# Kernel tuning notes

Measured on AMD Instinct MI355X. Metric: run time of the kernel, lower is better.

## Reference

```python
import jax, jax.numpy as jnp
import numpy as np

R, B, S, H, E = 8, 8, 512, 768, 64


def setup_inputs() -> dict:
    key = jax.random.key(0)
    ks = jax.random.split(key, 9)
    return {
        "role_labels": jax.random.uniform(ks[0], (R, B, S), dtype=jnp.float32),
        "summar_role_embedding": jax.random.normal(ks[1], (R, B, S, H), dtype=jnp.float32),
        "token_embedding": jax.random.normal(ks[2], (B, S, H), dtype=jnp.float32),
        "entities_embedding": jax.random.normal(ks[3], (B, S, H), dtype=jnp.float32),
        "token_mask": jnp.ones((B, S), jnp.float32),
        "entity2token": jax.random.randint(ks[4], (B, S), 0, E, dtype=jnp.int32),
        "token2entity": jax.random.randint(ks[5], (B, S), 0, E, dtype=jnp.int32),
        "W_single": jax.random.normal(ks[6], (3 * H, 1), dtype=jnp.float32) * 0.02,
        "b_single": jnp.zeros((1,), jnp.float32),
        "W_multi": jax.random.normal(ks[7], (3 * H, 1), dtype=jnp.float32) * 0.02,
        "b_multi": jnp.zeros((1,), jnp.float32),
        "W_ans": jax.random.normal(ks[8], (2 * H, H), dtype=jnp.float32) * 0.02,
        "b_ans": jnp.zeros((H,), jnp.float32),
    }


def reference(role_labels, summar_role_embedding, token_embedding, entities_embedding,
              token_mask, entity2token, token2entity,
              W_single, b_single, W_multi, b_multi, W_ans, b_ans):
    Bn = token_embedding.shape[0]
    # flattened segment ids: batch b, entity e -> b*E + e
    seg = (jnp.arange(Bn, dtype=entity2token.dtype)[:, None] * E + entity2token).reshape(-1)
    eps = 1e-7
    mask_sum = token_mask.sum()

    def step(carry, xs):
        pre_answer, loss = carry
        sr, labels = xs  # [B,S,H], [B,S]
        single = jax.nn.sigmoid(
            jnp.concatenate([sr, token_embedding, pre_answer], -1) @ W_single + b_single)[..., 0]
        multi = jax.nn.sigmoid(
            jnp.concatenate([sr, entities_embedding, pre_answer], -1) @ W_multi + b_multi)[..., 0]
        # per-(batch,entity) scatter-max of multi-word scores
        scores = jax.ops.segment_max(multi.reshape(-1), seg, num_segments=Bn * E).reshape(Bn, E)
        scores = jnp.maximum(scores, 0.0)  # entity_scores initialized to 0 in original
        # broadcast entity score back to its token span positions
        pred_ent = jnp.take_along_axis(scores, token2entity.astype(jnp.int32), axis=1)
        merged = jnp.maximum(single, pred_ent)  # [B,S]
        curr_answer = token_embedding * merged[..., None]
        pre_next = jnp.concatenate([curr_answer, pre_answer], -1) @ W_ans + b_ans
        p = jnp.clip(merged, eps, 1.0 - eps)
        bce = -(labels * jnp.log(p) + (1.0 - labels) * jnp.log1p(-p)).mean()
        loss = loss + bce * mask_sum  # (BCE-mean scalar * mask).sum() == bce * mask.sum()
        return (pre_next, loss), merged

    init = (jnp.zeros_like(token_embedding), jnp.asarray(0.0, jnp.float32))
    (_, total_loss), logits = jax.lax.scan(step, init, (summar_role_embedding, role_labels))
    return total_loss, logits  # scalar, [R,B,S]
```

## Files before the change

### kernel.cpp

```cpp
#include <hip/hip_runtime.h>
#include <math.h>

#define HD   768
#define NR   8
#define NB   8
#define SL   512
#define NE   64
#define NTOK 4096
#define NSR  32768

__device__ __forceinline__ float wred(float v) {
  #pragma unroll
  for (int m = 32; m >= 1; m >>= 1) v += __shfl_xor(v, m, 64);
  return v;
}

__device__ __forceinline__ float dot12(const float4 a0, const float4 a1, const float4 a2,
                                       const float* __restrict__ w, int lane) {
  const float4 w0 = *reinterpret_cast<const float4*>(w + lane * 4);
  const float4 w1 = *reinterpret_cast<const float4*>(w + 256 + lane * 4);
  const float4 w2 = *reinterpret_cast<const float4*>(w + 512 + lane * 4);
  float s = 0.f;
  s = fmaf(a0.x, w0.x, s); s = fmaf(a0.y, w0.y, s); s = fmaf(a0.z, w0.z, s); s = fmaf(a0.w, w0.w, s);
  s = fmaf(a1.x, w1.x, s); s = fmaf(a1.y, w1.y, s); s = fmaf(a1.z, w1.z, s); s = fmaf(a1.w, w1.w, s);
  s = fmaf(a2.x, w2.x, s); s = fmaf(a2.y, w2.y, s); s = fmaf(a2.z, w2.z, s); s = fmaf(a2.w, w2.w, s);
  return s;
}

__global__ __launch_bounds__(256) void chain_kernel(
    const float* __restrict__ W_ans, const float* __restrict__ b_ans,
    const float* __restrict__ uS_in, const float* __restrict__ uM_in,
    float* __restrict__ vS_out, float* __restrict__ vM_out,
    float* __restrict__ uS_out, float* __restrict__ uM_out,
    float* __restrict__ buS, float* __restrict__ buM)
{
  const int wid  = blockIdx.x * 4 + (threadIdx.x >> 6);
  const int lane = threadIdx.x & 63;
  if (wid < 3072) {
    const int cm  = (wid >= 1536);
    const int row = wid - (cm ? 1536 : 0);
    const float* u = cm ? uM_in : uS_in;
    const float* wr = W_ans + (size_t)row * HD;
    const float4 a0 = *reinterpret_cast<const float4*>(wr + lane * 4);
    const float4 a1 = *reinterpret_cast<const float4*>(wr + 256 + lane * 4);
    const float4 a2 = *reinterpret_cast<const float4*>(wr + 512 + lane * 4);
    float acc = wred(dot12(a0, a1, a2, u, lane));
    if (lane == 0) {
      if (row < HD) { (cm ? vM_out : vS_out)[row] = acc; }
      else          { (cm ? uM_out : uS_out)[row - HD] = acc; }
    }
  } else if (wid < 3074) {
    const float* u = (wid == 3073) ? uM_in : uS_in;
    const float4 a0 = *reinterpret_cast<const float4*>(b_ans + lane * 4);
    const float4 a1 = *reinterpret_cast<const float4*>(b_ans + 256 + lane * 4);
    const float4 a2 = *reinterpret_cast<const float4*>(b_ans + 512 + lane * 4);
    float acc = wred(dot12(a0, a1, a2, u, lane));
    if (lane == 0) { if (wid == 3073) *buM = acc; else *buS = acc; }
  }
}

__global__ __launch_bounds__(256) void dots_kernel(
    const float* __restrict__ sr, const float* __restrict__ tok, const float* __restrict__ ent,
    const float* __restrict__ Wsing, const float* __restrict__ Wmult,
    const float* __restrict__ vS, const float* __restrict__ vM,
    float* __restrict__ as_out, float* __restrict__ am_out,
    float* __restrict__ ps_out, float* __restrict__ pm_out,
    float* __restrict__ dts_out, float* __restrict__ dem_out)
{
  const int wid  = blockIdx.x * 4 + (threadIdx.x >> 6);
  const int lane = threadIdx.x & 63;
  if (wid < NSR) {
    const float* row = sr + (size_t)wid * HD;
    const float4 x0 = *reinterpret_cast<const float4*>(row + lane * 4);
    const float4 x1 = *reinterpret_cast<const float4*>(row + 256 + lane * 4);
    const float4 x2 = *reinterpret_cast<const float4*>(row + 512 + lane * 4);
    float aS = wred(dot12(x0, x1, x2, Wsing, lane));
    float aM = wred(dot12(x0, x1, x2, Wmult, lane));
    if (lane == 0) { as_out[wid] = aS; am_out[wid] = aM; }
  } else if (wid < NSR + NTOK) {
    const int t = wid - NSR;
    const float* tr = tok + (size_t)t * HD;
    const float* er = ent + (size_t)t * HD;
    const float4 t0 = *reinterpret_cast<const float4*>(tr + lane * 4);
    const float4 t1 = *reinterpret_cast<const float4*>(tr + 256 + lane * 4);
    const float4 t2 = *reinterpret_cast<const float4*>(tr + 512 + lane * 4);
    const float4 e0 = *reinterpret_cast<const float4*>(er + lane * 4);
    const float4 e1 = *reinterpret_cast<const float4*>(er + 256 + lane * 4);
    const float4 e2v = *reinterpret_cast<const float4*>(er + 512 + lane * 4);
    float dts = wred(dot12(t0, t1, t2, Wsing + HD, lane));
    float dem = wred(dot12(e0, e1, e2v, Wmult + HD, lane));
    float psv[7], pmv[7];
    #pragma unroll
    for (int k = 0; k < 7; ++k) {
      psv[k] = wred(dot12(t0, t1, t2, vS + k * HD, lane));
      pmv[k] = wred(dot12(t0, t1, t2, vM + k * HD, lane));
    }
    if (lane == 0) {
      dts_out[t] = dts; dem_out[t] = dem;
      #pragma unroll
      for (int k = 0; k < 7; ++k) { ps_out[k * NTOK + t] = psv[k]; pm_out[k * NTOK + t] = pmv[k]; }
    }
  }
}

__global__ __launch_bounds__(512) void step_kernel(
    const float* __restrict__ labels, const int* __restrict__ e2t, const int* __restrict__ t2e,
    const float* __restrict__ ps, const float* __restrict__ pm,
    const float* __restrict__ dts, const float* __restrict__ dem,
    const float* __restrict__ as_, const float* __restrict__ am_,
    const float* __restrict__ buS, const float* __restrict__ buM,
    const float* __restrict__ b_single, const float* __restrict__ b_multi,
    float* __restrict__ out, double* __restrict__ partial_bce)
{
  __shared__ unsigned sc[NR][NE];
  const int s = threadIdx.x;
  const int b = blockIdx.x;
  const int t = b * SL + s;
  reinterpret_cast<unsigned*>(sc)[s] = 0u;
  float psv[7], pmv[7], asv[8], amv[8], buSv[7], buMv[7];
  #pragma unroll
  for (int k = 0; k < 7; ++k) { psv[k] = ps[k * NTOK + t]; pmv[k] = pm[k * NTOK + t]; }
  #pragma unroll
  for (int r = 0; r < 8; ++r) { asv[r] = as_[r * NTOK + t]; amv[r] = am_[r * NTOK + t]; }
  #pragma unroll
  for (int k = 0; k < 7; ++k) { buSv[k] = buS[k]; buMv[k] = buM[k]; }
  const float dtsv = dts[t], demv = dem[t];
  const float b1 = b_single[0], b2 = b_multi[0];
  const int e2 = e2t[t] & (NE - 1);
  const int t2 = t2e[t] & (NE - 1);
  __syncthreads();

  float m[8];
  float cs = 0.f, cmv = 0.f;
  double bsum = 0.0;
  #pragma unroll
  for (int r = 0; r < 8; ++r) {
    float As = cs, Am = cmv;
    #pragma unroll
    for (int j = 0; j < r; ++j) {
      As = fmaf(m[j], psv[r - 1 - j], As);
      Am = fmaf(m[j], pmv[r - 1 - j], Am);
    }
    const float xs = asv[r] + dtsv + As + b1;
    const float xm = amv[r] + demv + Am + b2;
    const float sing = 1.f / (1.f + expf(-xs));
    const float mult = 1.f / (1.f + expf(-xm));
    atomicMax(&sc[r][e2], __float_as_uint(mult));
    __syncthreads();
    const float pred = __uint_as_float(sc[r][t2]);
    const float merged = fmaxf(sing, pred);
    m[r] = merged;
    out[1 + r * NTOK + t] = merged;
    const float lab = labels[r * NTOK + t];
    const float p = fminf(fmaxf(merged, 1e-7f), 1.0f - 1e-7f);
    bsum += (double)(-(lab * logf(p) + (1.f - lab) * log1pf(-p)));
    if (r < 7) { cs += buSv[r]; cmv += buMv[r]; }
  }
  #pragma unroll
  for (int off = 32; off >= 1; off >>= 1) bsum += __shfl_xor(bsum, off, 64);
  __shared__ double wsum[8];
  if ((threadIdx.x & 63) == 0) wsum[threadIdx.x >> 6] = bsum;
  __syncthreads();
  if (threadIdx.x == 0) {
    double tot = 0.0;
    #pragma unroll
    for (int i = 0; i < 8; ++i) tot += wsum[i];
    partial_bce[b] = tot;
  }
}

__global__ __launch_bounds__(256) void finalize_kernel(
    const float* __restrict__ mask, const double* __restrict__ partial_bce, float* __restrict__ out)
{
  const int tid = threadIdx.x;
  float sm = 0.f;
  for (int i = tid; i < NTOK; i += 256) sm += mask[i];
  sm = wred(sm);
  __shared__ float w4[4];
  if ((tid & 63) == 0) w4[tid >> 6] = sm;
  __syncthreads();
  if (tid == 0) {
    const float msum = w4[0] + w4[1] + w4[2] + w4[3];
    double tot = 0.0;
    #pragma unroll
    for (int i = 0; i < 8; ++i) tot += partial_bce[i];
    out[0] = (float)(tot * (double)msum / 4096.0);
  }
}

extern "C" void kernel_launch(void* const* d_in, const int* in_sizes, int n_in,
                              void* d_out, int out_size, void* d_ws, size_t ws_size,
                              hipStream_t stream) {
  (void)in_sizes; (void)n_in; (void)out_size; (void)ws_size;
  const float* labels = (const float*)d_in[0];
  const float* sr     = (const float*)d_in[1];
  const float* tok    = (const float*)d_in[2];
  const float* ent    = (const float*)d_in[3];
  const float* mask   = (const float*)d_in[4];
  const int*   e2t    = (const int*)d_in[5];
  const int*   t2e    = (const int*)d_in[6];
  const float* Wsing  = (const float*)d_in[7];
  const float* bsing  = (const float*)d_in[8];
  const float* Wmult  = (const float*)d_in[9];
  const float* bmult  = (const float*)d_in[10];
  const float* Wans   = (const float*)d_in[11];
  const float* bans   = (const float*)d_in[12];

  float* ws  = (float*)d_ws;
  float* uS  = ws;
  float* uM  = uS + 8 * HD;
  float* vS  = uM + 8 * HD;
  float* vM  = vS + 7 * HD;
  float* buS = vM + 7 * HD;
  float* buM = buS + 8;
  float* ps  = buM + 8;
  float* pm  = ps + 7 * NTOK;
  float* dts = pm + 7 * NTOK;
  float* dem = dts + NTOK;
  float* as_ = dem + NTOK;
  float* am_ = as_ + 8 * NTOK;
  double* pb = (double*)(am_ + 8 * NTOK);

  for (int k = 0; k < 7; ++k) {
    const float* uSin = (k == 0) ? (Wsing + 2 * HD) : (uS + k * HD);
    const float* uMin = (k == 0) ? (Wmult + 2 * HD) : (uM + k * HD);
    chain_kernel<<<769, 256, 0, stream>>>(Wans, bans, uSin, uMin,
        vS + k * HD, vM + k * HD, uS + (k + 1) * HD, uM + (k + 1) * HD,
        buS + k, buM + k);
  }
  dots_kernel<<<9216, 256, 0, stream>>>(sr, tok, ent, Wsing, Wmult, vS, vM,
        as_, am_, ps, pm, dts, dem);
  step_kernel<<<8, 512, 0, stream>>>(labels, e2t, t2e, ps, pm, dts, dem,
        as_, am_, buS, buM, bsing, bmult, (float*)d_out, pb);
  finalize_kernel<<<1, 256, 0, stream>>>(mask, pb, (float*)d_out);
}
```

Before: 234.7 us.

## Fuse all stages into one persistent kernel with grid barriers and overlapped sr dots

```diff
diff --git a/kernel.cpp b/kernel.cpp
--- a/kernel.cpp
+++ b/kernel.cpp
@@ -8,8 +8,26 @@
 #define NE   64
 #define NTOK 4096
 #define NSR  32768
+#define GRID 768
+#define NWAVES (GRID * 4)
+#define SRSLICE 4682
+#define C1N 16
+#define C1TARGET (GRID / C1N)
+
+struct Args {
+  const float *labels, *sr, *tok, *ent, *mask;
+  const int *e2t, *t2e;
+  const float *Wsing, *bsing, *Wmult, *bmult, *Wans, *bans;
+  float *ws;
+  float *out;
+};
 
 __device__ __forceinline__ float wred(float v) {
+  #pragma unroll
+  for (int m = 32; m >= 1; m >>= 1) v += __shfl_xor(v, m, 64);
+  return v;
+}
+__device__ __forceinline__ double wredd(double v) {
   #pragma unroll
   for (int m = 32; m >= 1; m >>= 1) v += __shfl_xor(v, m, 64);
   return v;
@@ -27,164 +45,196 @@
   return s;
 }
 
-__global__ __launch_bounds__(256) void chain_kernel(
-    const float* __restrict__ W_ans, const float* __restrict__ b_ans,
-    const float* __restrict__ uS_in, const float* __restrict__ uM_in,
-    float* __restrict__ vS_out, float* __restrict__ vM_out,
-    float* __restrict__ uS_out, float* __restrict__ uM_out,
-    float* __restrict__ buS, float* __restrict__ buM)
-{
-  const int wid  = blockIdx.x * 4 + (threadIdx.x >> 6);
-  const int lane = threadIdx.x & 63;
-  if (wid < 3072) {
-    const int cm  = (wid >= 1536);
-    const int row = wid - (cm ? 1536 : 0);
-    const float* u = cm ? uM_in : uS_in;
-    const float* wr = W_ans + (size_t)row * HD;
-    const float4 a0 = *reinterpret_cast<const float4*>(wr + lane * 4);
-    const float4 a1 = *reinterpret_cast<const float4*>(wr + 256 + lane * 4);
-    const float4 a2 = *reinterpret_cast<const float4*>(wr + 512 + lane * 4);
-    float acc = wred(dot12(a0, a1, a2, u, lane));
-    if (lane == 0) {
-      if (row < HD) { (cm ? vM_out : vS_out)[row] = acc; }
-      else          { (cm ? uM_out : uS_out)[row - HD] = acc; }
-    }
-  } else if (wid < 3074) {
-    const float* u = (wid == 3073) ? uM_in : uS_in;
-    const float4 a0 = *reinterpret_cast<const float4*>(b_ans + lane * 4);
-    const float4 a1 = *reinterpret_cast<const float4*>(b_ans + 256 + lane * 4);
-    const float4 a2 = *reinterpret_cast<const float4*>(b_ans + 512 + lane * 4);
-    float acc = wred(dot12(a0, a1, a2, u, lane));
-    if (lane == 0) { if (wid == 3073) *buM = acc; else *buS = acc; }
-  }
-}
-
-__global__ __launch_bounds__(256) void dots_kernel(
-    const float* __restrict__ sr, const float* __restrict__ tok, const float* __restrict__ ent,
-    const float* __restrict__ Wsing, const float* __restrict__ Wmult,
-    const float* __restrict__ vS, const float* __restrict__ vM,
-    float* __restrict__ as_out, float* __restrict__ am_out,
-    float* __restrict__ ps_out, float* __restrict__ pm_out,
-    float* __restrict__ dts_out, float* __restrict__ dem_out)
-{
-  const int wid  = blockIdx.x * 4 + (threadIdx.x >> 6);
-  const int lane = threadIdx.x & 63;
-  if (wid < NSR) {
-    const float* row = sr + (size_t)wid * HD;
-    const float4 x0 = *reinterpret_cast<const float4*>(row + lane * 4);
-    const float4 x1 = *reinterpret_cast<const float4*>(row + 256 + lane * 4);
-    const float4 x2 = *reinterpret_cast<const float4*>(row + 512 + lane * 4);
-    float aS = wred(dot12(x0, x1, x2, Wsing, lane));
-    float aM = wred(dot12(x0, x1, x2, Wmult, lane));
-    if (lane == 0) { as_out[wid] = aS; am_out[wid] = aM; }
-  } else if (wid < NSR + NTOK) {
-    const int t = wid - NSR;
-    const float* tr = tok + (size_t)t * HD;
-    const float* er = ent + (size_t)t * HD;
+__device__ __forceinline__ float rowdot(const float* __restrict__ a, const float* __restrict__ w, int lane) {
+  const float4 a0 = *reinterpret_cast<const float4*>(a + lane * 4);
+  const float4 a1 = *reinterpret_cast<const float4*>(a + 256 + lane * 4);
+  const float4 a2 = *reinterpret_cast<const float4*>(a + 512 + lane * 4);
+  return wred(dot12(a0, a1, a2, w, lane));
+}
+
+__device__ __forceinline__ void gridbar(unsigned* B, int bid, int tid) {
+  __syncthreads();
+  if (tid == 0) {
+    __threadfence();
+    unsigned* c1  = B + (bid & (C1N - 1)) * 32;
+    unsigned* c2  = B + 512;
+    unsigned* gen = B + 544;
+    unsigned g = __hip_atomic_load(gen, __ATOMIC_RELAXED, __HIP_MEMORY_SCOPE_AGENT);
+    bool done = false;
+    if (__hip_atomic_fetch_add(c1, 1u, __ATOMIC_ACQ_REL, __HIP_MEMORY_SCOPE_AGENT) == C1TARGET - 1) {
+      __hip_atomic_store(c1, 0u, __ATOMIC_RELAXED, __HIP_MEMORY_SCOPE_AGENT);
+      if (__hip_atomic_fetch_add(c2, 1u, __ATOMIC_ACQ_REL, __HIP_MEMORY_SCOPE_AGENT) == C1N - 1) {
+        __hip_atomic_store(c2, 0u, __ATOMIC_RELAXED, __HIP_MEMORY_SCOPE_AGENT);
+        __hip_atomic_fetch_add(gen, 1u, __ATOMIC_RELEASE, __HIP_MEMORY_SCOPE_AGENT);
+        done = true;
+      }
+    }
+    if (!done) {
+      while (__hip_atomic_load(gen, __ATOMIC_RELAXED, __HIP_MEMORY_SCOPE_AGENT) == g)
+        __builtin_amdgcn_s_sleep(2);
+    }
+    __threadfence();
+  }
+  __syncthreads();
+}
+
+__global__ void init_kernel(unsigned* B) {
+  for (int i = threadIdx.x; i < 640; i += 256) B[i] = 0u;
+}
+
+__global__ __launch_bounds__(256, 4) void fused_kernel(Args A) {
+  const int tid  = threadIdx.x;
+  const int lane = tid & 63;
+  const int bid  = blockIdx.x;
+  const int gwid = bid * 4 + (tid >> 6);
+
+  unsigned* B  = (unsigned*)A.ws;
+  float* F     = A.ws;
+  float* msum  = F + 640;
+  double* pbce = (double*)(F + 648);
+  float* uS  = F + 704;
+  float* uM  = uS + 8 * HD;
+  float* vS  = uM + 8 * HD;
+  float* vM  = vS + 7 * HD;
+  float* buS = vM + 7 * HD;
+  float* buM = buS + 8;
+  float* as_ = F + 24064;
+  float* am_ = as_ + NSR;
+  float* ps  = am_ + NSR;
+  float* pm  = ps + 7 * NTOK;
+  float* dts = pm + 7 * NTOK;
+  float* dem = dts + NTOK;
+
+  for (int p = 0; p < 7; ++p) {
+    if (gwid < 1536) {
+      const int cm  = gwid >= 768;
+      const int row = gwid & 767;
+      const float* u = (p == 0) ? ((cm ? A.Wmult : A.Wsing) + 2 * HD)
+                                : ((cm ? uM : uS) + p * HD);
+      if (p < 6) {
+        float acc = rowdot(A.Wans + (size_t)(HD + row) * HD, u, lane);
+        if (lane == 0) ((cm ? uM : uS) + (p + 1) * HD)[row] = acc;
+      }
+      if (row == 0) {
+        float bb = rowdot(A.bans, u, lane);
+        if (lane == 0) (cm ? buM : buS)[p] = bb;
+      }
+    } else if (gwid < 3072) {
+      const int cm  = gwid >= 2304;
+      const int row = gwid & 767;
+      const float* u = (p == 0) ? ((cm ? A.Wmult : A.Wsing) + 2 * HD)
+                                : ((cm ? uM : uS) + p * HD);
+      float acc = rowdot(A.Wans + (size_t)row * HD, u, lane);
+      if (lane == 0) ((cm ? vM : vS) + p * HD)[row] = acc;
+    }
+    if (p == 0 && gwid == 1600) {
+      const float4* m4 = (const float4*)A.mask;
+      float sm = 0.f;
+      for (int i = lane; i < NTOK / 4; i += 64) {
+        float4 v = m4[i];
+        sm += v.x + v.y + v.z + v.w;
+      }
+      sm = wred(sm);
+      if (lane == 0) *msum = sm;
+    }
+    const int e = ((p + 1) * SRSLICE < NSR) ? (p + 1) * SRSLICE : NSR;
+    for (int r = p * SRSLICE + gwid; r < e; r += NWAVES) {
+      const float* row = A.sr + (size_t)r * HD;
+      const float4 x0 = *reinterpret_cast<const float4*>(row + lane * 4);
+      const float4 x1 = *reinterpret_cast<const float4*>(row + 256 + lane * 4);
+      const float4 x2 = *reinterpret_cast<const float4*>(row + 512 + lane * 4);
+      float aS = wred(dot12(x0, x1, x2, A.Wsing, lane));
+      float aM = wred(dot12(x0, x1, x2, A.Wmult, lane));
+      if (lane == 0) { as_[r] = aS; am_[r] = aM; }
+    }
+    gridbar(B, bid, tid);
+  }
+
+  for (int t = gwid; t < NTOK; t += NWAVES) {
+    const float* tr = A.tok + (size_t)t * HD;
+    const float* er = A.ent + (size_t)t * HD;
     const float4 t0 = *reinterpret_cast<const float4*>(tr + lane * 4);
     const float4 t1 = *reinterpret_cast<const float4*>(tr + 256 + lane * 4);
     const float4 t2 = *reinterpret_cast<const float4*>(tr + 512 + lane * 4);
     const float4 e0 = *reinterpret_cast<const float4*>(er + lane * 4);
     const float4 e1 = *reinterpret_cast<const float4*>(er + 256 + lane * 4);
-    const float4 e2v = *reinterpret_cast<const float4*>(er + 512 + lane * 4);
-    float dts = wred(dot12(t0, t1, t2, Wsing + HD, lane));
-    float dem = wred(dot12(e0, e1, e2v, Wmult + HD, lane));
-    float psv[7], pmv[7];
+    const float4 e2 = *reinterpret_cast<const float4*>(er + 512 + lane * 4);
+    float dtsv = wred(dot12(t0, t1, t2, A.Wsing + HD, lane));
+    float demv = wred(dot12(e0, e1, e2, A.Wmult + HD, lane));
+    if (lane == 0) { dts[t] = dtsv; dem[t] = demv; }
     #pragma unroll
     for (int k = 0; k < 7; ++k) {
-      psv[k] = wred(dot12(t0, t1, t2, vS + k * HD, lane));
-      pmv[k] = wred(dot12(t0, t1, t2, vM + k * HD, lane));
-    }
-    if (lane == 0) {
-      dts_out[t] = dts; dem_out[t] = dem;
-      #pragma unroll
-      for (int k = 0; k < 7; ++k) { ps_out[k * NTOK + t] = psv[k]; pm_out[k * NTOK + t] = pmv[k]; }
-    }
-  }
-}
-
-__global__ __launch_bounds__(512) void step_kernel(
-    const float* __restrict__ labels, const int* __restrict__ e2t, const int* __restrict__ t2e,
-    const float* __restrict__ ps, const float* __restrict__ pm,
-    const float* __restrict__ dts, const float* __restrict__ dem,
-    const float* __restrict__ as_, const float* __restrict__ am_,
-    const float* __restrict__ buS, const float* __restrict__ buM,
-    const float* __restrict__ b_single, const float* __restrict__ b_multi,
-    float* __restrict__ out, double* __restrict__ partial_bce)
-{
+      float a = wred(dot12(t0, t1, t2, vS + k * HD, lane));
+      float b = wred(dot12(t0, t1, t2, vM + k * HD, lane));
+      if (lane == 0) { ps[k * NTOK + t] = a; pm[k * NTOK + t] = b; }
+    }
+  }
+  gridbar(B, bid, tid);
+
+  if (bid >= NB) return;
   __shared__ unsigned sc[NR][NE];
-  const int s = threadIdx.x;
-  const int b = blockIdx.x;
-  const int t = b * SL + s;
-  reinterpret_cast<unsigned*>(sc)[s] = 0u;
-  float psv[7], pmv[7], asv[8], amv[8], buSv[7], buMv[7];
-  #pragma unroll
-  for (int k = 0; k < 7; ++k) { psv[k] = ps[k * NTOK + t]; pmv[k] = pm[k * NTOK + t]; }
-  #pragma unroll
-  for (int r = 0; r < 8; ++r) { asv[r] = as_[r * NTOK + t]; amv[r] = am_[r * NTOK + t]; }
-  #pragma unroll
-  for (int k = 0; k < 7; ++k) { buSv[k] = buS[k]; buMv[k] = buM[k]; }
-  const float dtsv = dts[t], demv = dem[t];
-  const float b1 = b_single[0], b2 = b_multi[0];
-  const int e2 = e2t[t] & (NE - 1);
-  const int t2 = t2e[t] & (NE - 1);
-  __syncthreads();
-
-  float m[8];
+  __shared__ double wsumD[4];
+  const int b = bid;
+  const int t0 = b * SL + tid, t1 = t0 + 256;
+  reinterpret_cast<unsigned*>(sc)[tid] = 0u;
+  reinterpret_cast<unsigned*>(sc)[tid + 256] = 0u;
+  float ps0[7], pm0[7], ps1[7], pm1[7], buSv[7], buMv[7];
+  #pragma unroll
+  for (int k = 0; k < 7; ++k) {
+    ps0[k] = ps[k * NTOK + t0]; pm0[k] = pm[k * NTOK + t0];
+    ps1[k] = ps[k * NTOK + t1]; pm1[k] = pm[k * NTOK + t1];
+    buSv[k] = buS[k]; buMv[k] = buM[k];
+  }
+  const float dts0 = dts[t0], dem0 = dem[t0], dts1 = dts[t1], dem1 = dem[t1];
+  const float b1 = A.bsing[0], b2 = A.bmult[0];
+  const int e0i = A.e2t[t0] & (NE - 1), e1i = A.e2t[t1] & (NE - 1);
+  const int q0 = A.t2e[t0] & (NE - 1), q1 = A.t2e[t1] & (NE - 1);
+  __syncthreads();
+
+  float m0[8], m1[8];
   float cs = 0.f, cmv = 0.f;
   double bsum = 0.0;
   #pragma unroll
   for (int r = 0; r < 8; ++r) {
-    float As = cs, Am = cmv;
+    float As0 = cs, Am0 = cmv, As1 = cs, Am1 = cmv;
     #pragma unroll
     for (int j = 0; j < r; ++j) {
-      As = fmaf(m[j], psv[r - 1 - j], As);
-      Am = fmaf(m[j], pmv[r - 1 - j], Am);
-    }
-    const float xs = asv[r] + dtsv + As + b1;
-    const float xm = amv[r] + demv + Am + b2;
-    const float sing = 1.f / (1.f + expf(-xs));
-    const float mult = 1.f / (1.f + expf(-xm));
-    atomicMax(&sc[r][e2], __float_as_uint(mult));
+      As0 = fmaf(m0[j], ps0[r - 1 - j], As0); Am0 = fmaf(m0[j], pm0[r - 1 - j], Am0);
+      As1 = fmaf(m1[j], ps1[r - 1 - j], As1); Am1 = fmaf(m1[j], pm1[r - 1 - j], Am1);
+    }
+    const float sing0 = 1.f / (1.f + expf(-(as_[r * NTOK + t0] + dts0 + As0 + b1)));
+    const float mult0 = 1.f / (1.f + expf(-(am_[r * NTOK + t0] + dem0 + Am0 + b2)));
+    const float sing1 = 1.f / (1.f + expf(-(as_[r * NTOK + t1] + dts1 + As1 + b1)));
+    const float mult1 = 1.f / (1.f + expf(-(am_[r * NTOK + t1] + dem1 + Am1 + b2)));
+    atomicMax(&sc[r][e0i], __float_as_uint(mult0));
+    atomicMax(&sc[r][e1i], __float_as_uint(mult1));
     __syncthreads();
-    const float pred = __uint_as_float(sc[r][t2]);
-    const float merged = fmaxf(sing, pred);
-    m[r] = merged;
-    out[1 + r * NTOK + t] = merged;
-    const float lab = labels[r * NTOK + t];
-    const float p = fminf(fmaxf(merged, 1e-7f), 1.0f - 1e-7f);
-    bsum += (double)(-(lab * logf(p) + (1.f - lab) * log1pf(-p)));
+    const float mg0 = fmaxf(sing0, __uint_as_float(sc[r][q0]));
+    const float mg1 = fmaxf(sing1, __uint_as_float(sc[r][q1]));
+    m0[r] = mg0; m1[r] = mg1;
+    A.out[1 + r * NTOK + t0] = mg0;
+    A.out[1 + r * NTOK + t1] = mg1;
+    const float la0 = A.labels[r * NTOK + t0], la1 = A.labels[r * NTOK + t1];
+    const float p0 = fminf(fmaxf(mg0, 1e-7f), 1.f - 1e-7f);
+    const float p1 = fminf(fmaxf(mg1, 1e-7f), 1.f - 1e-7f);
+    bsum += (double)(-(la0 * logf(p0) + (1.f - la0) * log1pf(-p0)));
+    bsum += (double)(-(la1 * logf(p1) + (1.f - la1) * log1pf(-p1)));
     if (r < 7) { cs += buSv[r]; cmv += buMv[r]; }
   }
-  #pragma unroll
-  for (int off = 32; off >= 1; off >>= 1) bsum += __shfl_xor(bsum, off, 64);
-  __shared__ double wsum[8];
-  if ((threadIdx.x & 63) == 0) wsum[threadIdx.x >> 6] = bsum;
-  __syncthreads();
-  if (threadIdx.x == 0) {
-    double tot = 0.0;
-    #pragma unroll
-    for (int i = 0; i < 8; ++i) tot += wsum[i];
-    partial_bce[b] = tot;
-  }
-}
-
-__global__ __launch_bounds__(256) void finalize_kernel(
-    const float* __restrict__ mask, const double* __restrict__ partial_bce, float* __restrict__ out)
-{
-  const int tid = threadIdx.x;
-  float sm = 0.f;
-  for (int i = tid; i < NTOK; i += 256) sm += mask[i];
-  sm = wred(sm);
-  __shared__ float w4[4];
-  if ((tid & 63) == 0) w4[tid >> 6] = sm;
+  bsum = wredd(bsum);
+  if ((tid & 63) == 0) wsumD[tid >> 6] = bsum;
   __syncthreads();
   if (tid == 0) {
-    const float msum = w4[0] + w4[1] + w4[2] + w4[3];
-    double tot = 0.0;
-    #pragma unroll
-    for (int i = 0; i < 8; ++i) tot += partial_bce[i];
-    out[0] = (float)(tot * (double)msum / 4096.0);
+    pbce[b] = wsumD[0] + wsumD[1] + wsumD[2] + wsumD[3];
+    __threadfence();
+    unsigned k = atomicAdd(B + 576, 1u);
+    if (k == NB - 1) {
+      __threadfence();
+      double tot = 0.0;
+      #pragma unroll
+      for (int i = 0; i < 8; ++i) tot += ((volatile double*)pbce)[i];
+      A.out[0] = (float)(tot * (double)(*(volatile float*)msum) / 4096.0);
+    }
   }
 }
 
@@ -192,45 +242,22 @@
                               void* d_out, int out_size, void* d_ws, size_t ws_size,
                               hipStream_t stream) {
   (void)in_sizes; (void)n_in; (void)out_size; (void)ws_size;
-  const float* labels = (const float*)d_in[0];
-  const float* sr     = (const float*)d_in[1];
-  const float* tok    = (const float*)d_in[2];
-  const float* ent    = (const float*)d_in[3];
-  const float* mask   = (const float*)d_in[4];
-  const int*   e2t    = (const int*)d_in[5];
-  const int*   t2e    = (const int*)d_in[6];
-  const float* Wsing  = (const float*)d_in[7];
-  const float* bsing  = (const float*)d_in[8];
-  const float* Wmult  = (const float*)d_in[9];
-  const float* bmult  = (const float*)d_in[10];
-  const float* Wans   = (const float*)d_in[11];
-  const float* bans   = (const float*)d_in[12];
-
-  float* ws  = (float*)d_ws;
-  float* uS  = ws;
-  float* uM  = uS + 8 * HD;
-  float* vS  = uM + 8 * HD;
-  float* vM  = vS + 7 * HD;
-  float* buS = vM + 7 * HD;
-  float* buM = buS + 8;
-  float* ps  = buM + 8;
-  float* pm  = ps + 7 * NTOK;
-  float* dts = pm + 7 * NTOK;
-  float* dem = dts + NTOK;
-  float* as_ = dem + NTOK;
-  float* am_ = as_ + 8 * NTOK;
-  double* pb = (double*)(am_ + 8 * NTOK);
-
-  for (int k = 0; k < 7; ++k) {
-    const float* uSin = (k == 0) ? (Wsing + 2 * HD) : (uS + k * HD);
-    const float* uMin = (k == 0) ? (Wmult + 2 * HD) : (uM + k * HD);
-    chain_kernel<<<769, 256, 0, stream>>>(Wans, bans, uSin, uMin,
-        vS + k * HD, vM + k * HD, uS + (k + 1) * HD, uM + (k + 1) * HD,
-        buS + k, buM + k);
-  }
-  dots_kernel<<<9216, 256, 0, stream>>>(sr, tok, ent, Wsing, Wmult, vS, vM,
-        as_, am_, ps, pm, dts, dem);
-  step_kernel<<<8, 512, 0, stream>>>(labels, e2t, t2e, ps, pm, dts, dem,
-        as_, am_, buS, buM, bsing, bmult, (float*)d_out, pb);
-  finalize_kernel<<<1, 256, 0, stream>>>(mask, pb, (float*)d_out);
-}
+  Args a;
+  a.labels = (const float*)d_in[0];
+  a.sr     = (const float*)d_in[1];
+  a.tok    = (const float*)d_in[2];
+  a.ent    = (const float*)d_in[3];
+  a.mask   = (const float*)d_in[4];
+  a.e2t    = (const int*)d_in[5];
+  a.t2e    = (const int*)d_in[6];
+  a.Wsing  = (const float*)d_in[7];
+  a.bsing  = (const float*)d_in[8];
+  a.Wmult  = (const float*)d_in[9];
+  a.bmult  = (const float*)d_in[10];
+  a.Wans   = (const float*)d_in[11];
+  a.bans   = (const float*)d_in[12];
+  a.ws     = (float*)d_ws;
+  a.out    = (float*)d_out;
+  init_kernel<<<1, 256, 0, stream>>>((unsigned*)d_ws);
+  fused_kernel<<<GRID, 256, 0, stream>>>(a);
+}
```

After: 630.5 us. 2.69x slower.
